# Performance work log

Hardware: AMD Instinct MI355X
Metric: run time of the kernel (lower is better)

The kernel has to match this reference:

```python
import jax, jax.numpy as jnp
import numpy as np

N = 100000          # nodes
E = 800000          # edges
H = 32              # hidden_features
L = 4               # num_layers
HS = 32             # hidden_edge_scores
EPS_BN = 1e-5
EPS_AGG = 1e-6


def _bn(x, g, b):
    # training-mode batch norm over the node/edge (batch) axis
    mu = jnp.mean(x, axis=0)
    var = jnp.var(x, axis=0)
    return (x - mu) * jax.lax.rsqrt(var + EPS_BN) * g + b


def setup_inputs() -> dict:
    key = jax.random.key(0)
    ks = jax.random.split(key, 24)
    rn = lambda k, s, sc=0.1: jax.random.normal(k, s, dtype=jnp.float32) * sc
    return {
        "x": rn(ks[0], (N, 1), 1.0),
        "e": rn(ks[1], (E, 1), 1.0),
        "edge_index": jax.random.randint(ks[2], (2, E), 0, N),
        # input projections
        "pe_w": rn(ks[3], (1, H)), "pe_b": rn(ks[4], (H,)),
        "ed_w": rn(ks[5], (1, H)), "ed_b": rn(ks[6], (H,)),
        # per-layer GatedGCN weights, stacked over layers
        "A_w": rn(ks[7], (L, H, H)), "A_b": rn(ks[8], (L, H)),
        "B_w": rn(ks[9], (L, H, H)), "B_b": rn(ks[10], (L, H)),
        "C_w": rn(ks[11], (L, H, H)), "C_b": rn(ks[12], (L, H)),
        "U_w": rn(ks[13], (L, H, H)), "U_b": rn(ks[14], (L, H)),
        "V_w": rn(ks[15], (L, H, H)), "V_b": rn(ks[16], (L, H)),
        # batch-norm affine params
        "bn_h_g": jnp.ones((L, H), jnp.float32), "bn_h_b": jnp.zeros((L, H), jnp.float32),
        "bn_e_g": jnp.ones((L, H), jnp.float32), "bn_e_b": jnp.zeros((L, H), jnp.float32),
        # score predictor: concat(src_h, dst_h, e) -> HS -> 1
        "W1_w": rn(ks[17], (3 * H, HS)), "W1_b": rn(ks[18], (HS,)),
        "W2_w": rn(ks[19], (HS, 1)), "W2_b": rn(ks[20], (1,)),
    }


def reference(x, e, edge_index, pe_w, pe_b, ed_w, ed_b,
              A_w, A_b, B_w, B_b, C_w, C_b, U_w, U_b, V_w, V_b,
              bn_h_g, bn_h_b, bn_e_g, bn_e_b, W1_w, W1_b, W2_w, W2_b):
    src, dst = edge_index[0], edge_index[1]
    h = x @ pe_w + pe_b          # [N, H]
    e = e @ ed_w + ed_b          # [E, H]
    n = h.shape[0]
    for l in range(L):
        Ah = h @ A_w[l] + A_b[l]
        Bh = h @ B_w[l] + B_b[l]
        Ce = e @ C_w[l] + C_b[l]
        Uh = h @ U_w[l] + U_b[l]
        Vh = h @ V_w[l] + V_b[l]
        # edge update: gather node features to edges
        e_new = Ah[dst] + Bh[src] + Ce               # [E, H]
        sigma = jax.nn.sigmoid(e_new)                # edge gates
        # gated mean aggregation: scatter-add to dst nodes
        num = jax.ops.segment_sum(sigma * Vh[src], dst, num_segments=n)
        den = jax.ops.segment_sum(sigma, dst, num_segments=n)
        h_new = Uh + num / (den + EPS_AGG)           # [N, H]
        # BN -> ReLU -> residual
        h = h + jax.nn.relu(_bn(h_new, bn_h_g[l], bn_h_b[l]))
        e = e + jax.nn.relu(_bn(e_new, bn_e_g[l], bn_e_b[l]))
    # score predictor over edges
    z = jnp.concatenate([h[src], h[dst], e], axis=1)  # [E, 3H]
    scores = jax.nn.relu(z @ W1_w + W1_b) @ W2_w + W2_b  # [E, 1]
    return scores
```

## Files before the change

kernel.cpp:

```cpp
#include <hip/hip_runtime.h>
#include <hip/hip_bf16.h>
#include <hip/hip_fp16.h>

#define NLAYERS 4
#define GRID_STRIDE 2048

typedef _Float16 half8_t __attribute__((ext_vector_type(8)));
typedef float float4_t __attribute__((ext_vector_type(4)));
typedef float float8_t __attribute__((ext_vector_type(8)));

__global__ void zero_ints(int* __restrict__ p, int n)
{
    int i = blockIdx.x * 256 + threadIdx.x;
    if (i < n) p[i] = 0;
}

__global__ void hist_kernel(const int* __restrict__ dsts, int* __restrict__ counts, int E)
{
    int i = blockIdx.x * 256 + threadIdx.x;
    if (i < E) atomicAdd(&counts[dsts[i]], 1);
}

__global__ __launch_bounds__(256) void scan1(const int* __restrict__ counts,
                                             int* __restrict__ offsets,
                                             int* __restrict__ blocksums, int N)
{
    __shared__ int sdata[256];
    int t = threadIdx.x;
    int bbase = blockIdx.x * 1024;
    int v[4]; int s = 0;
#pragma unroll
    for (int q = 0; q < 4; q++) {
        int idx = bbase + t * 4 + q;
        v[q] = (idx < N) ? counts[idx] : 0;
        s += v[q];
    }
    sdata[t] = s;
    __syncthreads();
    for (int off = 1; off < 256; off <<= 1) {
        int x = (t >= off) ? sdata[t - off] : 0;
        __syncthreads();
        sdata[t] += x;
        __syncthreads();
    }
    int excl = sdata[t] - s;
    int run = excl;
#pragma unroll
    for (int q = 0; q < 4; q++) {
        int idx = bbase + t * 4 + q;
        if (idx < N) offsets[idx] = run;
        run += v[q];
    }
    if (t == 255) blocksums[blockIdx.x] = sdata[255];
}

__global__ void scan2(int* __restrict__ blocksums, int nb)
{
    if (threadIdx.x == 0 && blockIdx.x == 0) {
        int run = 0;
        for (int b = 0; b < nb; b++) { int t = blocksums[b]; blocksums[b] = run; run += t; }
    }
}

__global__ void scan3(int* __restrict__ offsets, const int* __restrict__ blocksums,
                      int* __restrict__ cursor, int N)
{
    int i = blockIdx.x * 256 + threadIdx.x;
    if (i < N) {
        int v = offsets[i] + blocksums[i >> 10];
        offsets[i] = v;
        cursor[i] = v;
    }
}

__global__ void scatter_perm(const int* __restrict__ dsts, int* __restrict__ cursor,
                             int* __restrict__ perm, int* __restrict__ pos, int E, int N)
{
    int g = blockIdx.x & 7;
    int lo = (int)((long long)N * g >> 3);
    int hi = (int)((long long)N * (g + 1) >> 3);
    int nbg = gridDim.x >> 3;
    int bg = blockIdx.x >> 3;
    for (int i = bg * 256 + threadIdx.x; i < E; i += nbg * 256) {
        int d = dsts[i];
        if (d >= lo && d < hi) {
            int slot = atomicAdd(&cursor[d], 1);
            perm[slot] = i;
            pos[i] = slot;
        }
    }
}

__global__ void gather_sd(const int* __restrict__ perm, const int* __restrict__ srcs,
                          const int* __restrict__ dsts, int* __restrict__ srcp,
                          int* __restrict__ dstp, int E)
{
    int i = blockIdx.x * 256 + threadIdx.x;
    if (i < E) {
        int e = perm[i];
        srcp[i] = srcs[e];
        dstp[i] = dsts[e];
    }
}

__global__ void init_proj4(const float* __restrict__ in, const float* __restrict__ w,
                           const float* __restrict__ b, float4* __restrict__ out, size_t n4)
{
    size_t i = (size_t)blockIdx.x * 256 + threadIdx.x;
    if (i < n4) {
        int j4 = (int)(i & 7) * 4;
        float xv = in[i >> 3];
        float4 wv = *(const float4*)(w + j4);
        float4 bv = *(const float4*)(b + j4);
        out[i] = make_float4(fmaf(xv, wv.x, bv.x), fmaf(xv, wv.y, bv.y),
                             fmaf(xv, wv.z, bv.z), fmaf(xv, wv.w, bv.w));
    }
}

__global__ void init_ep16(const float* __restrict__ e_in, const int* __restrict__ perm,
                          const float* __restrict__ w, const float* __restrict__ b,
                          __half2* __restrict__ out, size_t n4)
{
    size_t i = (size_t)blockIdx.x * 256 + threadIdx.x;
    if (i < n4) {
        int row = (int)(i >> 3);
        float xv = e_in[perm[row]];
        int j4 = (int)(i & 7) * 4;
        float4 wv = *(const float4*)(w + j4);
        float4 bv = *(const float4*)(b + j4);
        out[i * 2]     = __floats2half2_rn(fmaf(xv, wv.x, bv.x), fmaf(xv, wv.y, bv.y));
        out[i * 2 + 1] = __floats2half2_rn(fmaf(xv, wv.z, bv.z), fmaf(xv, wv.w, bv.w));
    }
}

template <int FUSE>
__global__ __launch_bounds__(256) void node_gemm(
    float* __restrict__ h, const float* __restrict__ hnew_in,
    const float* __restrict__ sc_h, const float* __restrict__ sh_h,
    const float* __restrict__ Aw, const float* __restrict__ Ab,
    const float* __restrict__ Bw, const float* __restrict__ Bb,
    const float* __restrict__ Uw, const float* __restrict__ Ub,
    const float* __restrict__ Vw, const float* __restrict__ Vb,
    __half* __restrict__ Ahh, __half* __restrict__ Bhh,
    float* __restrict__ Uhh, __half* __restrict__ Vhh, int N)
{
    int tid = threadIdx.x;
    int lane = tid & 63;
    int m = lane & 15, q = lane >> 4;
    half8_t bA0, bA1, bB0, bB1, bU0, bU1, bV0, bV1;
    float scq[8], shq[8];
#pragma unroll
    for (int i = 0; i < 8; i++) {
        int k = q * 8 + i;
        bA0[i] = (_Float16)Aw[k * 32 + m];  bA1[i] = (_Float16)Aw[k * 32 + m + 16];
        bB0[i] = (_Float16)Bw[k * 32 + m];  bB1[i] = (_Float16)Bw[k * 32 + m + 16];
        bU0[i] = (_Float16)Uw[k * 32 + m];  bU1[i] = (_Float16)Uw[k * 32 + m + 16];
        bV0[i] = (_Float16)Vw[k * 32 + m];  bV1[i] = (_Float16)Vw[k * 32 + m + 16];
        if (FUSE) { scq[i] = sc_h[k]; shq[i] = sh_h[k]; }
    }
    float ab0 = Ab[m], ab1 = Ab[m + 16];
    float bb0 = Bb[m], bb1 = Bb[m + 16];
    float ub0 = Ub[m], ub1 = Ub[m + 16];
    float vb0 = Vb[m], vb1 = Vb[m + 16];

    int ntile = (N + 15) >> 4;
    int wid = blockIdx.x * 4 + (tid >> 6);
    int nwave = gridDim.x * 4;
    for (int t = wid; t < ntile; t += nwave) {
        int base = t << 4;
        int arow = base + m;
        bool valid = arow < N;
        if (!valid) arow = N - 1;
        float8_t hv = *(const float8_t*)(h + (size_t)arow * 32 + q * 8);
        if (FUSE) {
            float8_t pv = *(const float8_t*)(hnew_in + (size_t)arow * 32 + q * 8);
#pragma unroll
            for (int i = 0; i < 8; i++)
                hv[i] += fmaxf(fmaf(pv[i], scq[i], shq[i]), 0.f);
            if (valid) *(float8_t*)(h + (size_t)arow * 32 + q * 8) = hv;
        }
        half8_t a;
#pragma unroll
        for (int i = 0; i < 8; i++) a[i] = (_Float16)hv[i];
        float4_t aA0 = __builtin_amdgcn_mfma_f32_16x16x32_f16(a, bA0, (float4_t){0,0,0,0}, 0, 0, 0);
        float4_t aA1 = __builtin_amdgcn_mfma_f32_16x16x32_f16(a, bA1, (float4_t){0,0,0,0}, 0, 0, 0);
        float4_t aB0 = __builtin_amdgcn_mfma_f32_16x16x32_f16(a, bB0, (float4_t){0,0,0,0}, 0, 0, 0);
        float4_t aB1 = __builtin_amdgcn_mfma_f32_16x16x32_f16(a, bB1, (float4_t){0,0,0,0}, 0, 0, 0);
        float4_t aU0 = __builtin_amdgcn_mfma_f32_16x16x32_f16(a, bU0, (float4_t){0,0,0,0}, 0, 0, 0);
        float4_t aU1 = __builtin_amdgcn_mfma_f32_16x16x32_f16(a, bU1, (float4_t){0,0,0,0}, 0, 0, 0);
        float4_t aV0 = __builtin_amdgcn_mfma_f32_16x16x32_f16(a, bV0, (float4_t){0,0,0,0}, 0, 0, 0);
        float4_t aV1 = __builtin_amdgcn_mfma_f32_16x16x32_f16(a, bV1, (float4_t){0,0,0,0}, 0, 0, 0);
#pragma unroll
        for (int reg = 0; reg < 4; reg++) {
            int node = base + q * 4 + reg;
            if (node < N) {
                size_t o = (size_t)node * 32;
                Ahh[o + m]      = __float2half_rn(aA0[reg] + ab0);
                Ahh[o + m + 16] = __float2half_rn(aA1[reg] + ab1);
                Bhh[o + m]      = __float2half_rn(aB0[reg] + bb0);
                Bhh[o + m + 16] = __float2half_rn(aB1[reg] + bb1);
                Vhh[o + m]      = __float2half_rn(aV0[reg] + vb0);
                Vhh[o + m + 16] = __float2half_rn(aV1[reg] + vb1);
                Uhh[o + m]      = aU0[reg] + ub0;
                Uhh[o + m + 16] = aU1[reg] + ub1;
            }
        }
    }
}

__global__ __launch_bounds__(256) void edge_en(
    const __half* __restrict__ ep,
    const int* __restrict__ srcp, const int* __restrict__ dstp,
    const __half* __restrict__ Ah, const __half* __restrict__ Bh,
    const float* __restrict__ Cw, const float* __restrict__ Cb,
    __half* __restrict__ enh, float* __restrict__ partial, int E)
{
    __shared__ float red[256];
    int tid = threadIdx.x;
    int lane = tid & 63;
    int m = lane & 15, q = lane >> 4;
    half8_t b0, b1;
#pragma unroll
    for (int i = 0; i < 8; i++) {
        int k = q * 8 + i;
        b0[i] = (_Float16)Cw[k * 32 + m];
        b1[i] = (_Float16)Cw[k * 32 + m + 16];
    }
    float cb0 = Cb[m], cb1 = Cb[m + 16];
    float es0 = 0.f, eq0 = 0.f, es1 = 0.f, eq1 = 0.f;

    int ntile = (E + 15) >> 4;
    int wid = blockIdx.x * 4 + (tid >> 6);
    int nwave = gridDim.x * 4;
    for (int t = wid; t < ntile; t += nwave) {
        int base = t << 4;
        int arow = base + m;
        if (arow >= E) arow = E - 1;
        half8_t a = *(const half8_t*)(ep + (size_t)arow * 32 + q * 8);
        float4_t acc0 = __builtin_amdgcn_mfma_f32_16x16x32_f16(a, b0, (float4_t){0.f,0.f,0.f,0.f}, 0, 0, 0);
        float4_t acc1 = __builtin_amdgcn_mfma_f32_16x16x32_f16(a, b1, (float4_t){0.f,0.f,0.f,0.f}, 0, 0, 0);
#pragma unroll
        for (int reg = 0; reg < 4; reg++) {
            int row = q * 4 + reg;
            int edge = base + row;
            if (edge < E) {
                int s = srcp[edge], d = dstp[edge];
                float ah0 = __half2float(Ah[(size_t)d * 32 + m]);
                float bh0 = __half2float(Bh[(size_t)s * 32 + m]);
                float ah1 = __half2float(Ah[(size_t)d * 32 + m + 16]);
                float bh1 = __half2float(Bh[(size_t)s * 32 + m + 16]);
                float en0 = acc0[reg] + cb0 + ah0 + bh0;
                float en1 = acc1[reg] + cb1 + ah1 + bh1;
                enh[(size_t)edge * 32 + m]      = __float2half_rn(en0);
                enh[(size_t)edge * 32 + m + 16] = __float2half_rn(en1);
                es0 += en0; eq0 += en0 * en0;
                es1 += en1; eq1 += en1 * en1;
            }
        }
    }
    float* p = partial + (size_t)blockIdx.x * 64;
    __syncthreads();
    red[tid] = es0;
    __syncthreads();
    if (tid < 16) {
        float s = 0.f;
#pragma unroll
        for (int w = 0; w < 4; w++)
#pragma unroll
            for (int k = 0; k < 4; k++) s += red[w * 64 + k * 16 + tid];
        p[tid] = s;
    }
    __syncthreads();
    red[tid] = es1;
    __syncthreads();
    if (tid < 16) {
        float s = 0.f;
#pragma unroll
        for (int w = 0; w < 4; w++)
#pragma unroll
            for (int k = 0; k < 4; k++) s += red[w * 64 + k * 16 + tid];
        p[16 + tid] = s;
    }
    __syncthreads();
    red[tid] = eq0;
    __syncthreads();
    if (tid < 16) {
        float s = 0.f;
#pragma unroll
        for (int w = 0; w < 4; w++)
#pragma unroll
            for (int k = 0; k < 4; k++) s += red[w * 64 + k * 16 + tid];
        p[32 + tid] = s;
    }
    __syncthreads();
    red[tid] = eq1;
    __syncthreads();
    if (tid < 16) {
        float s = 0.f;
#pragma unroll
        for (int w = 0; w < 4; w++)
#pragma unroll
            for (int k = 0; k < 4; k++) s += red[w * 64 + k * 16 + tid];
        p[48 + tid] = s;
    }
}

__global__ __launch_bounds__(256) void node_agg(
    const __half* __restrict__ enh, const int* __restrict__ srcp,
    const int* __restrict__ offsets, const int* __restrict__ counts,
    const __half* __restrict__ Vh, float* __restrict__ hnew,
    __half* __restrict__ ep, const float* __restrict__ sc_e, const float* __restrict__ sh_e,
    float* __restrict__ partial, int N)
{
    __shared__ float red[512];
    int tid = threadIdx.x, u = tid & 15, grp = tid >> 4;
    int c0 = 2 * u;
    float sc0 = sc_e[c0], sh0 = sh_e[c0];
    float sc1 = sc_e[c0 + 1], sh1 = sh_e[c0 + 1];
    float hs0 = 0.f, hq0 = 0.f, hs1 = 0.f, hq1 = 0.f;
    for (int nb0 = blockIdx.x * 16; nb0 < N; nb0 += gridDim.x * 16) {
        int node = nb0 + grp;
        if (node >= N) break;
        int start = offsets[node], len = counts[node];
        float num0 = 0.f, den0 = 0.f, num1 = 0.f, den1 = 0.f;
        int qq = 0;
        for (; qq + 2 <= len; qq += 2) {
            int p0 = start + qq, p1 = p0 + 1;
            int s0 = srcp[p0], s1 = srcp[p1];
            float2 en0 = __half22float2(*(const __half2*)(enh + (size_t)p0 * 32 + c0));
            float2 en1 = __half22float2(*(const __half2*)(enh + (size_t)p1 * 32 + c0));
            float2 vh0 = __half22float2(*(const __half2*)(Vh + (size_t)s0 * 32 + c0));
            float2 vh1 = __half22float2(*(const __half2*)(Vh + (size_t)s1 * 32 + c0));
            float2 e0 = __half22float2(*(const __half2*)(ep + (size_t)p0 * 32 + c0));
            float2 e1 = __half22float2(*(const __half2*)(ep + (size_t)p1 * 32 + c0));
            float sg00 = 1.f / (1.f + __expf(-en0.x)), sg01 = 1.f / (1.f + __expf(-en0.y));
            float sg10 = 1.f / (1.f + __expf(-en1.x)), sg11 = 1.f / (1.f + __expf(-en1.y));
            num0 = fmaf(sg00, vh0.x, num0); num1 = fmaf(sg01, vh0.y, num1);
            num0 = fmaf(sg10, vh1.x, num0); num1 = fmaf(sg11, vh1.y, num1);
            den0 += sg00 + sg10; den1 += sg01 + sg11;
            *(__half2*)(ep + (size_t)p0 * 32 + c0) = __floats2half2_rn(
                e0.x + fmaxf(fmaf(en0.x, sc0, sh0), 0.f),
                e0.y + fmaxf(fmaf(en0.y, sc1, sh1), 0.f));
            *(__half2*)(ep + (size_t)p1 * 32 + c0) = __floats2half2_rn(
                e1.x + fmaxf(fmaf(en1.x, sc0, sh0), 0.f),
                e1.y + fmaxf(fmaf(en1.y, sc1, sh1), 0.f));
        }
        if (qq < len) {
            int p0 = start + qq;
            int s0 = srcp[p0];
            float2 en0 = __half22float2(*(const __half2*)(enh + (size_t)p0 * 32 + c0));
            float2 vh0 = __half22float2(*(const __half2*)(Vh + (size_t)s0 * 32 + c0));
            float2 e0 = __half22float2(*(const __half2*)(ep + (size_t)p0 * 32 + c0));
            float sg00 = 1.f / (1.f + __expf(-en0.x)), sg01 = 1.f / (1.f + __expf(-en0.y));
            num0 = fmaf(sg00, vh0.x, num0); num1 = fmaf(sg01, vh0.y, num1);
            den0 += sg00; den1 += sg01;
            *(__half2*)(ep + (size_t)p0 * 32 + c0) = __floats2half2_rn(
                e0.x + fmaxf(fmaf(en0.x, sc0, sh0), 0.f),
                e0.y + fmaxf(fmaf(en0.y, sc1, sh1), 0.f));
        }
        size_t ho = (size_t)node * 32 + c0;
        float hv0 = hnew[ho]     + num0 / (den0 + 1e-6f);
        float hv1 = hnew[ho + 1] + num1 / (den1 + 1e-6f);
        *(float2*)(hnew + ho) = make_float2(hv0, hv1);
        hs0 += hv0; hq0 += hv0 * hv0;
        hs1 += hv1; hq1 += hv1 * hv1;
    }
    __syncthreads();
    red[tid] = hs0; red[256 + tid] = hs1;
    __syncthreads();
    float* p = partial + (size_t)blockIdx.x * 64;
    if (tid < 32) {
        int uu = tid >> 1, par = tid & 1;
        const float* r = red + par * 256;
        float s = 0.f;
#pragma unroll
        for (int g = 0; g < 16; g++) s += r[g * 16 + uu];
        p[tid] = s;
    }
    __syncthreads();
    red[tid] = hq0; red[256 + tid] = hq1;
    __syncthreads();
    if (tid < 32) {
        int uu = tid >> 1, par = tid & 1;
        const float* r = red + par * 256;
        float s = 0.f;
#pragma unroll
        for (int g = 0; g < 16; g++) s += r[g * 16 + uu];
        p[32 + tid] = s;
    }
}

__global__ __launch_bounds__(256) void stats_side(
    const float* __restrict__ partial, int nrows, double cnt,
    const float* __restrict__ g, const float* __restrict__ b,
    float* __restrict__ sc_out, float* __restrict__ sh_out)
{
    int j = blockIdx.x;
    __shared__ double rs[256], rq[256];
    double s = 0.0, q = 0.0;
    for (int r = threadIdx.x; r < nrows; r += 256) {
        s += (double)partial[(size_t)r * 64 + j];
        q += (double)partial[(size_t)r * 64 + 32 + j];
    }
    rs[threadIdx.x] = s; rq[threadIdx.x] = q;
    __syncthreads();
    for (int off = 128; off; off >>= 1) {
        if (threadIdx.x < off) { rs[threadIdx.x] += rs[threadIdx.x + off]; rq[threadIdx.x] += rq[threadIdx.x + off]; }
        __syncthreads();
    }
    if (threadIdx.x == 0) {
        double mean = rs[0] / cnt;
        double var = rq[0] / cnt - mean * mean;
        float scale = g[j] * (float)(1.0 / sqrt(var + 1e-5));
        sc_out[j] = scale;
        sh_out[j] = b[j] - (float)mean * scale;
    }
}

__global__ void apply4_h16(const float4* __restrict__ pre, const float* __restrict__ scale,
                           const float* __restrict__ shift, const float4* __restrict__ hold,
                           __half2* __restrict__ h16, size_t n4)
{
    size_t i = (size_t)blockIdx.x * 256 + threadIdx.x;
    if (i < n4) {
        int j4 = (int)(i & 7) * 4;
        float4 sc = *(const float4*)(scale + j4);
        float4 sh = *(const float4*)(shift + j4);
        float4 p = pre[i], a = hold[i];
        a.x += fmaxf(fmaf(p.x, sc.x, sh.x), 0.f);
        a.y += fmaxf(fmaf(p.y, sc.y, sh.y), 0.f);
        a.z += fmaxf(fmaf(p.z, sc.z, sh.z), 0.f);
        a.w += fmaxf(fmaf(p.w, sc.w, sh.w), 0.f);
        h16[i * 2]     = __floats2half2_rn(a.x, a.y);
        h16[i * 2 + 1] = __floats2half2_rn(a.z, a.w);
    }
}

__global__ __launch_bounds__(256) void predictor(
    const __half* __restrict__ h16, const __half* __restrict__ e16,
    const int* __restrict__ srcs, const int* __restrict__ dsts, const int* __restrict__ pos,
    const float* __restrict__ W1, const float* __restrict__ b1,
    const float* __restrict__ W2, const float* __restrict__ b2v,
    float* __restrict__ out, int E)
{
    int tid = threadIdx.x;
    int lane = tid & 63;
    int m = lane & 15, q = lane >> 4;
    half8_t bf00, bf01, bf10, bf11, bf20, bf21;
#pragma unroll
    for (int i = 0; i < 8; i++) {
        int k = q * 8 + i;
        bf00[i] = (_Float16)W1[k * 32 + m];
        bf01[i] = (_Float16)W1[k * 32 + m + 16];
        bf10[i] = (_Float16)W1[(32 + k) * 32 + m];
        bf11[i] = (_Float16)W1[(32 + k) * 32 + m + 16];
        bf20[i] = (_Float16)W1[(64 + k) * 32 + m];
        bf21[i] = (_Float16)W1[(64 + k) * 32 + m + 16];
    }
    float b10 = b1[m], b11 = b1[m + 16];
    float w20 = W2[m], w21 = W2[m + 16];
    float b2 = b2v[0];

    int ntile = (E + 15) >> 4;
    int wid = blockIdx.x * 4 + (tid >> 6);
    int nwave = gridDim.x * 4;
    for (int t = wid; t < ntile; t += nwave) {
        int base = t << 4;
        int arow = base + m;
        if (arow >= E) arow = E - 1;
        int s = srcs[arow], d = dsts[arow];
        int erow = pos[arow];
        half8_t a0 = *(const half8_t*)(h16 + (size_t)s * 32 + q * 8);
        half8_t a1 = *(const half8_t*)(h16 + (size_t)d * 32 + q * 8);
        half8_t a2 = *(const half8_t*)(e16 + (size_t)erow * 32 + q * 8);
        float4_t acc0 = {0.f, 0.f, 0.f, 0.f}, acc1 = {0.f, 0.f, 0.f, 0.f};
        acc0 = __builtin_amdgcn_mfma_f32_16x16x32_f16(a0, bf00, acc0, 0, 0, 0);
        acc1 = __builtin_amdgcn_mfma_f32_16x16x32_f16(a0, bf01, acc1, 0, 0, 0);
        acc0 = __builtin_amdgcn_mfma_f32_16x16x32_f16(a1, bf10, acc0, 0, 0, 0);
        acc1 = __builtin_amdgcn_mfma_f32_16x16x32_f16(a1, bf11, acc1, 0, 0, 0);
        acc0 = __builtin_amdgcn_mfma_f32_16x16x32_f16(a2, bf20, acc0, 0, 0, 0);
        acc1 = __builtin_amdgcn_mfma_f32_16x16x32_f16(a2, bf21, acc1, 0, 0, 0);
#pragma unroll
        for (int reg = 0; reg < 4; reg++) {
            float tp = fmaxf(acc0[reg] + b10, 0.f) * w20
                     + fmaxf(acc1[reg] + b11, 0.f) * w21;
            tp += __shfl_xor(tp, 1);
            tp += __shfl_xor(tp, 2);
            tp += __shfl_xor(tp, 4);
            tp += __shfl_xor(tp, 8);
            int edge = base + q * 4 + reg;
            if (m == 0 && edge < E) out[edge] = tp + b2;
        }
    }
}

extern "C" void kernel_launch(void* const* d_in, const int* in_sizes, int n_in,
                              void* d_out, int out_size, void* d_ws, size_t ws_size,
                              hipStream_t stream)
{
    const int N = in_sizes[0];
    const int E = in_sizes[1];

    const float* x    = (const float*)d_in[0];
    const float* e_in = (const float*)d_in[1];
    const int*   eidx = (const int*)d_in[2];
    const float* pe_w = (const float*)d_in[3];
    const float* pe_b = (const float*)d_in[4];
    const float* ed_w = (const float*)d_in[5];
    const float* ed_b = (const float*)d_in[6];
    const float* Aw = (const float*)d_in[7];
    const float* Ab = (const float*)d_in[8];
    const float* Bw = (const float*)d_in[9];
    const float* Bb = (const float*)d_in[10];
    const float* Cw = (const float*)d_in[11];
    const float* Cb = (const float*)d_in[12];
    const float* Uw = (const float*)d_in[13];
    const float* Ub = (const float*)d_in[14];
    const float* Vw = (const float*)d_in[15];
    const float* Vb = (const float*)d_in[16];
    const float* bn_h_g = (const float*)d_in[17];
    const float* bn_h_b = (const float*)d_in[18];
    const float* bn_e_g = (const float*)d_in[19];
    const float* bn_e_b = (const float*)d_in[20];
    const float* W1w = (const float*)d_in[21];
    const float* W1b = (const float*)d_in[22];
    const float* W2w = (const float*)d_in[23];
    const float* W2b = (const float*)d_in[24];

    const int* srcs = eidx;
    const int* dsts = eidx + E;

    size_t nh = (size_t)N * 32;
    size_t eh = (size_t)E * 32;

    float* ws = (float*)d_ws;
    float* stats     = ws;
    float* partial_h = stats + 128;
    float* partial_e = partial_h + GRID_STRIDE * 64;
    float* h    = partial_e + GRID_STRIDE * 64;
    float* hnew = h + nh;
    __half* Ah  = (__half*)(hnew + nh);
    __half* Bh  = Ah + nh;
    __half* Vh  = Bh + nh;
    __half* ep  = Vh + nh;
    __half* enh = ep + eh;
    int* counts    = (int*)(enh + eh);
    int* offsets   = counts + N;
    int* cursor    = offsets + N;
    int* blocksums = cursor + N;
    int* perm      = blocksums + 128;
    int* srcp      = perm + E;
    int* dstp      = srcp + E;
    int* pos       = dstp + E;

    size_t nh4 = nh / 4, eh4 = eh / 4;
    int gh4 = (int)((nh4 + 255) / 256);
    int ge4 = (int)((eh4 + 255) / 256);
    int gN = (N + 255) / 256;
    int gE = (E + 255) / 256;
    int nb = (N + 1023) / 1024;
    int ntileN = (N + 15) / 16;
    int gGemm = (ntileN + 3) / 4;
    if (gGemm > GRID_STRIDE) gGemm = GRID_STRIDE;

    zero_ints<<<gN, 256, 0, stream>>>(counts, N);
    hist_kernel<<<gE, 256, 0, stream>>>(dsts, counts, E);
    scan1<<<nb, 256, 0, stream>>>(counts, offsets, blocksums, N);
    scan2<<<1, 64, 0, stream>>>(blocksums, nb);
    scan3<<<gN, 256, 0, stream>>>(offsets, blocksums, cursor, N);
    scatter_perm<<<GRID_STRIDE, 256, 0, stream>>>(dsts, cursor, perm, pos, E, N);
    gather_sd<<<gE, 256, 0, stream>>>(perm, srcs, dsts, srcp, dstp, E);

    init_proj4<<<gh4, 256, 0, stream>>>(x, pe_w, pe_b, (float4*)h, nh4);
    init_ep16<<<ge4, 256, 0, stream>>>(e_in, perm, ed_w, ed_b, (__half2*)ep, eh4);

    for (int l = 0; l < NLAYERS; l++) {
        if (l == 0)
            node_gemm<0><<<gGemm, 256, 0, stream>>>(h, hnew, stats + 0, stats + 32,
                Aw + l * 1024, Ab + l * 32, Bw + l * 1024, Bb + l * 32,
                Uw + l * 1024, Ub + l * 32, Vw + l * 1024, Vb + l * 32,
                Ah, Bh, hnew, Vh, N);
        else
            node_gemm<1><<<gGemm, 256, 0, stream>>>(h, hnew, stats + 0, stats + 32,
                Aw + l * 1024, Ab + l * 32, Bw + l * 1024, Bb + l * 32,
                Uw + l * 1024, Ub + l * 32, Vw + l * 1024, Vb + l * 32,
                Ah, Bh, hnew, Vh, N);
        edge_en<<<GRID_STRIDE, 256, 0, stream>>>(ep, srcp, dstp, Ah, Bh,
            Cw + l * 1024, Cb + l * 32, enh, partial_e, E);
        stats_side<<<32, 256, 0, stream>>>(partial_e, GRID_STRIDE, (double)E,
            bn_e_g + l * 32, bn_e_b + l * 32, stats + 64, stats + 96);
        node_agg<<<GRID_STRIDE, 256, 0, stream>>>(enh, srcp, offsets, counts,
            Vh, hnew, ep, stats + 64, stats + 96, partial_h, N);
        stats_side<<<32, 256, 0, stream>>>(partial_h, GRID_STRIDE, (double)N,
            bn_h_g + l * 32, bn_h_b + l * 32, stats + 0, stats + 32);
    }

    apply4_h16<<<gh4, 256, 0, stream>>>((const float4*)hnew, stats + 0, stats + 32,
                                        (const float4*)h, (__half2*)Ah, nh4);

    predictor<<<GRID_STRIDE, 256, 0, stream>>>((const __half*)Ah, (const __half*)ep,
                                               srcs, dsts, pos, W1w, W1b, W2w, W2b,
                                               (float*)d_out, E);
}
```

Baseline: 714.1 us.

## Fuse edge update and node aggregation into one dst-sorted kernel with deferred edge BN

Merges the per-edge C-projection and the gated aggregation into one kernel that walks dst-sorted edges per node. The edge residual update from the previous layer's BN is deferred and applied while the next layer reads the edge features; the last layer's update is applied inside the predictor. B and V are interleaved into one buffer so a single source gather fetches both, and the two stats kernels per layer become one. The aim is to cut enh/ep memory round-trips, the dstp index stream and launches. In exchange the Ce GEMM moves from MFMA to scalar FMAs driven by shuffles, which adds ALU work per edge.

```diff
diff --git a/kernel.cpp b/kernel.cpp
--- a/kernel.cpp
+++ b/kernel.cpp
@@ -91,16 +91,11 @@
     }
 }
 
-__global__ void gather_sd(const int* __restrict__ perm, const int* __restrict__ srcs,
-                          const int* __restrict__ dsts, int* __restrict__ srcp,
-                          int* __restrict__ dstp, int E)
+__global__ void gather_s(const int* __restrict__ perm, const int* __restrict__ srcs,
+                         int* __restrict__ srcp, int E)
 {
     int i = blockIdx.x * 256 + threadIdx.x;
-    if (i < E) {
-        int e = perm[i];
-        srcp[i] = srcs[e];
-        dstp[i] = dsts[e];
-    }
+    if (i < E) srcp[i] = srcs[perm[i]];
 }
 
 __global__ void init_proj4(const float* __restrict__ in, const float* __restrict__ w,
@@ -141,8 +136,8 @@
     const float* __restrict__ Bw, const float* __restrict__ Bb,
     const float* __restrict__ Uw, const float* __restrict__ Ub,
     const float* __restrict__ Vw, const float* __restrict__ Vb,
-    __half* __restrict__ Ahh, __half* __restrict__ Bhh,
-    float* __restrict__ Uhh, __half* __restrict__ Vhh, int N)
+    __half* __restrict__ Ahh, __half* __restrict__ BVh,
+    float* __restrict__ Uhh, int N)
 {
     int tid = threadIdx.x;
     int lane = tid & 63;
@@ -194,191 +189,111 @@
         for (int reg = 0; reg < 4; reg++) {
             int node = base + q * 4 + reg;
             if (node < N) {
-                size_t o = (size_t)node * 32;
-                Ahh[o + m]      = __float2half_rn(aA0[reg] + ab0);
-                Ahh[o + m + 16] = __float2half_rn(aA1[reg] + ab1);
-                Bhh[o + m]      = __float2half_rn(aB0[reg] + bb0);
-                Bhh[o + m + 16] = __float2half_rn(aB1[reg] + bb1);
-                Vhh[o + m]      = __float2half_rn(aV0[reg] + vb0);
-                Vhh[o + m + 16] = __float2half_rn(aV1[reg] + vb1);
-                Uhh[o + m]      = aU0[reg] + ub0;
-                Uhh[o + m + 16] = aU1[reg] + ub1;
+                size_t o  = (size_t)node * 32;
+                size_t o2 = (size_t)node * 64;
+                Ahh[o + m]       = __float2half_rn(aA0[reg] + ab0);
+                Ahh[o + m + 16]  = __float2half_rn(aA1[reg] + ab1);
+                BVh[o2 + m]      = __float2half_rn(aB0[reg] + bb0);
+                BVh[o2 + m + 16] = __float2half_rn(aB1[reg] + bb1);
+                BVh[o2 + 32 + m] = __float2half_rn(aV0[reg] + vb0);
+                BVh[o2 + 48 + m] = __float2half_rn(aV1[reg] + vb1);
+                Uhh[o + m]       = aU0[reg] + ub0;
+                Uhh[o + m + 16]  = aU1[reg] + ub1;
             }
         }
     }
 }
 
-__global__ __launch_bounds__(256) void edge_en(
-    const __half* __restrict__ ep,
-    const int* __restrict__ srcp, const int* __restrict__ dstp,
-    const __half* __restrict__ Ah, const __half* __restrict__ Bh,
+template <int FIRST>
+__global__ __launch_bounds__(256) void fused_edge_node(
+    const int* __restrict__ srcp, const int* __restrict__ offsets,
+    const int* __restrict__ counts,
+    const __half* __restrict__ Ahh, const __half* __restrict__ BVh,
+    __half* __restrict__ ep, __half* __restrict__ enh,
     const float* __restrict__ Cw, const float* __restrict__ Cb,
-    __half* __restrict__ enh, float* __restrict__ partial, int E)
-{
-    __shared__ float red[256];
-    int tid = threadIdx.x;
-    int lane = tid & 63;
-    int m = lane & 15, q = lane >> 4;
-    half8_t b0, b1;
-#pragma unroll
-    for (int i = 0; i < 8; i++) {
-        int k = q * 8 + i;
-        b0[i] = (_Float16)Cw[k * 32 + m];
-        b1[i] = (_Float16)Cw[k * 32 + m + 16];
-    }
-    float cb0 = Cb[m], cb1 = Cb[m + 16];
-    float es0 = 0.f, eq0 = 0.f, es1 = 0.f, eq1 = 0.f;
-
-    int ntile = (E + 15) >> 4;
-    int wid = blockIdx.x * 4 + (tid >> 6);
-    int nwave = gridDim.x * 4;
-    for (int t = wid; t < ntile; t += nwave) {
-        int base = t << 4;
-        int arow = base + m;
-        if (arow >= E) arow = E - 1;
-        half8_t a = *(const half8_t*)(ep + (size_t)arow * 32 + q * 8);
-        float4_t acc0 = __builtin_amdgcn_mfma_f32_16x16x32_f16(a, b0, (float4_t){0.f,0.f,0.f,0.f}, 0, 0, 0);
-        float4_t acc1 = __builtin_amdgcn_mfma_f32_16x16x32_f16(a, b1, (float4_t){0.f,0.f,0.f,0.f}, 0, 0, 0);
-#pragma unroll
-        for (int reg = 0; reg < 4; reg++) {
-            int row = q * 4 + reg;
-            int edge = base + row;
-            if (edge < E) {
-                int s = srcp[edge], d = dstp[edge];
-                float ah0 = __half2float(Ah[(size_t)d * 32 + m]);
-                float bh0 = __half2float(Bh[(size_t)s * 32 + m]);
-                float ah1 = __half2float(Ah[(size_t)d * 32 + m + 16]);
-                float bh1 = __half2float(Bh[(size_t)s * 32 + m + 16]);
-                float en0 = acc0[reg] + cb0 + ah0 + bh0;
-                float en1 = acc1[reg] + cb1 + ah1 + bh1;
-                enh[(size_t)edge * 32 + m]      = __float2half_rn(en0);
-                enh[(size_t)edge * 32 + m + 16] = __float2half_rn(en1);
-                es0 += en0; eq0 += en0 * en0;
-                es1 += en1; eq1 += en1 * en1;
-            }
-        }
-    }
-    float* p = partial + (size_t)blockIdx.x * 64;
-    __syncthreads();
-    red[tid] = es0;
-    __syncthreads();
-    if (tid < 16) {
-        float s = 0.f;
-#pragma unroll
-        for (int w = 0; w < 4; w++)
-#pragma unroll
-            for (int k = 0; k < 4; k++) s += red[w * 64 + k * 16 + tid];
-        p[tid] = s;
-    }
-    __syncthreads();
-    red[tid] = es1;
-    __syncthreads();
-    if (tid < 16) {
-        float s = 0.f;
-#pragma unroll
-        for (int w = 0; w < 4; w++)
-#pragma unroll
-            for (int k = 0; k < 4; k++) s += red[w * 64 + k * 16 + tid];
-        p[16 + tid] = s;
-    }
-    __syncthreads();
-    red[tid] = eq0;
-    __syncthreads();
-    if (tid < 16) {
-        float s = 0.f;
-#pragma unroll
-        for (int w = 0; w < 4; w++)
-#pragma unroll
-            for (int k = 0; k < 4; k++) s += red[w * 64 + k * 16 + tid];
-        p[32 + tid] = s;
-    }
-    __syncthreads();
-    red[tid] = eq1;
-    __syncthreads();
-    if (tid < 16) {
-        float s = 0.f;
-#pragma unroll
-        for (int w = 0; w < 4; w++)
-#pragma unroll
-            for (int k = 0; k < 4; k++) s += red[w * 64 + k * 16 + tid];
-        p[48 + tid] = s;
-    }
-}
-
-__global__ __launch_bounds__(256) void node_agg(
-    const __half* __restrict__ enh, const int* __restrict__ srcp,
-    const int* __restrict__ offsets, const int* __restrict__ counts,
-    const __half* __restrict__ Vh, float* __restrict__ hnew,
-    __half* __restrict__ ep, const float* __restrict__ sc_e, const float* __restrict__ sh_e,
-    float* __restrict__ partial, int N)
+    const float* __restrict__ sc_e, const float* __restrict__ sh_e,
+    float* __restrict__ hnew, float* __restrict__ partial, int N)
 {
     __shared__ float red[512];
     int tid = threadIdx.x, u = tid & 15, grp = tid >> 4;
     int c0 = 2 * u;
-    float sc0 = sc_e[c0], sh0 = sh_e[c0];
-    float sc1 = sc_e[c0 + 1], sh1 = sh_e[c0 + 1];
+    float4 cw[16];
+#pragma unroll
+    for (int t = 0; t < 16; t++) {
+        float2 w0 = *(const float2*)(Cw + (2 * t) * 32 + c0);
+        float2 w1 = *(const float2*)(Cw + (2 * t + 1) * 32 + c0);
+        cw[t] = make_float4(w0.x, w0.y, w1.x, w1.y);
+    }
+    float cb0 = Cb[c0], cb1 = Cb[c0 + 1];
+    float sce0 = 0.f, she0 = 0.f, sce1 = 0.f, she1 = 0.f;
+    if (!FIRST) {
+        sce0 = sc_e[c0];     she0 = sh_e[c0];
+        sce1 = sc_e[c0 + 1]; she1 = sh_e[c0 + 1];
+    }
+    float es0 = 0.f, eq0 = 0.f, es1 = 0.f, eq1 = 0.f;
     float hs0 = 0.f, hq0 = 0.f, hs1 = 0.f, hq1 = 0.f;
+
     for (int nb0 = blockIdx.x * 16; nb0 < N; nb0 += gridDim.x * 16) {
         int node = nb0 + grp;
         if (node >= N) break;
         int start = offsets[node], len = counts[node];
+        float2 ah = __half22float2(*(const __half2*)(Ahh + (size_t)node * 32 + c0));
+        float base0 = cb0 + ah.x, base1 = cb1 + ah.y;
         float num0 = 0.f, den0 = 0.f, num1 = 0.f, den1 = 0.f;
-        int qq = 0;
-        for (; qq + 2 <= len; qq += 2) {
-            int p0 = start + qq, p1 = p0 + 1;
-            int s0 = srcp[p0], s1 = srcp[p1];
-            float2 en0 = __half22float2(*(const __half2*)(enh + (size_t)p0 * 32 + c0));
-            float2 en1 = __half22float2(*(const __half2*)(enh + (size_t)p1 * 32 + c0));
-            float2 vh0 = __half22float2(*(const __half2*)(Vh + (size_t)s0 * 32 + c0));
-            float2 vh1 = __half22float2(*(const __half2*)(Vh + (size_t)s1 * 32 + c0));
-            float2 e0 = __half22float2(*(const __half2*)(ep + (size_t)p0 * 32 + c0));
-            float2 e1 = __half22float2(*(const __half2*)(ep + (size_t)p1 * 32 + c0));
-            float sg00 = 1.f / (1.f + __expf(-en0.x)), sg01 = 1.f / (1.f + __expf(-en0.y));
-            float sg10 = 1.f / (1.f + __expf(-en1.x)), sg11 = 1.f / (1.f + __expf(-en1.y));
-            num0 = fmaf(sg00, vh0.x, num0); num1 = fmaf(sg01, vh0.y, num1);
-            num0 = fmaf(sg10, vh1.x, num0); num1 = fmaf(sg11, vh1.y, num1);
-            den0 += sg00 + sg10; den1 += sg01 + sg11;
-            *(__half2*)(ep + (size_t)p0 * 32 + c0) = __floats2half2_rn(
-                e0.x + fmaxf(fmaf(en0.x, sc0, sh0), 0.f),
-                e0.y + fmaxf(fmaf(en0.y, sc1, sh1), 0.f));
-            *(__half2*)(ep + (size_t)p1 * 32 + c0) = __floats2half2_rn(
-                e1.x + fmaxf(fmaf(en1.x, sc0, sh0), 0.f),
-                e1.y + fmaxf(fmaf(en1.y, sc1, sh1), 0.f));
-        }
-        if (qq < len) {
-            int p0 = start + qq;
-            int s0 = srcp[p0];
-            float2 en0 = __half22float2(*(const __half2*)(enh + (size_t)p0 * 32 + c0));
-            float2 vh0 = __half22float2(*(const __half2*)(Vh + (size_t)s0 * 32 + c0));
-            float2 e0 = __half22float2(*(const __half2*)(ep + (size_t)p0 * 32 + c0));
-            float sg00 = 1.f / (1.f + __expf(-en0.x)), sg01 = 1.f / (1.f + __expf(-en0.y));
-            num0 = fmaf(sg00, vh0.x, num0); num1 = fmaf(sg01, vh0.y, num1);
-            den0 += sg00; den1 += sg01;
-            *(__half2*)(ep + (size_t)p0 * 32 + c0) = __floats2half2_rn(
-                e0.x + fmaxf(fmaf(en0.x, sc0, sh0), 0.f),
-                e0.y + fmaxf(fmaf(en0.y, sc1, sh1), 0.f));
+        for (int qq = 0; qq < len; qq++) {
+            int p = start + qq;
+            int s = srcp[p];
+            const __half2* bv = (const __half2*)(BVh + (size_t)s * 64);
+            float2 bh = __half22float2(bv[u]);
+            float2 vh = __half22float2(bv[16 + u]);
+            float2 ev = __half22float2(*(const __half2*)(ep + (size_t)p * 32 + c0));
+            if (!FIRST) {
+                float2 enp = __half22float2(*(const __half2*)(enh + (size_t)p * 32 + c0));
+                ev.x += fmaxf(fmaf(enp.x, sce0, she0), 0.f);
+                ev.y += fmaxf(fmaf(enp.y, sce1, she1), 0.f);
+                *(__half2*)(ep + (size_t)p * 32 + c0) = __floats2half2_rn(ev.x, ev.y);
+            }
+            float a0 = base0 + bh.x, a1 = base1 + bh.y;
+#pragma unroll
+            for (int t = 0; t < 16; t++) {
+                float e0 = __shfl(ev.x, t, 16);
+                float e1 = __shfl(ev.y, t, 16);
+                a0 = fmaf(e0, cw[t].x, a0);
+                a0 = fmaf(e1, cw[t].z, a0);
+                a1 = fmaf(e0, cw[t].y, a1);
+                a1 = fmaf(e1, cw[t].w, a1);
+            }
+            *(__half2*)(enh + (size_t)p * 32 + c0) = __floats2half2_rn(a0, a1);
+            es0 += a0; eq0 += a0 * a0;
+            es1 += a1; eq1 += a1 * a1;
+            float sg0 = 1.f / (1.f + __expf(-a0));
+            float sg1 = 1.f / (1.f + __expf(-a1));
+            num0 = fmaf(sg0, vh.x, num0); num1 = fmaf(sg1, vh.y, num1);
+            den0 += sg0; den1 += sg1;
         }
         size_t ho = (size_t)node * 32 + c0;
-        float hv0 = hnew[ho]     + num0 / (den0 + 1e-6f);
-        float hv1 = hnew[ho + 1] + num1 / (den1 + 1e-6f);
+        float2 uh = *(const float2*)(hnew + ho);
+        float hv0 = uh.x + num0 / (den0 + 1e-6f);
+        float hv1 = uh.y + num1 / (den1 + 1e-6f);
         *(float2*)(hnew + ho) = make_float2(hv0, hv1);
         hs0 += hv0; hq0 += hv0 * hv0;
         hs1 += hv1; hq1 += hv1 * hv1;
     }
-    __syncthreads();
-    red[tid] = hs0; red[256 + tid] = hs1;
-    __syncthreads();
-    float* p = partial + (size_t)blockIdx.x * 64;
+
+    float* pp = partial + (size_t)blockIdx.x * 128;
+    __syncthreads();
+    red[tid] = es0; red[256 + tid] = es1;
+    __syncthreads();
     if (tid < 32) {
         int uu = tid >> 1, par = tid & 1;
         const float* r = red + par * 256;
         float s = 0.f;
 #pragma unroll
         for (int g = 0; g < 16; g++) s += r[g * 16 + uu];
-        p[tid] = s;
-    }
-    __syncthreads();
-    red[tid] = hq0; red[256 + tid] = hq1;
+        pp[tid] = s;
+    }
+    __syncthreads();
+    red[tid] = eq0; red[256 + tid] = eq1;
     __syncthreads();
     if (tid < 32) {
         int uu = tid >> 1, par = tid & 1;
@@ -386,21 +301,46 @@
         float s = 0.f;
 #pragma unroll
         for (int g = 0; g < 16; g++) s += r[g * 16 + uu];
-        p[32 + tid] = s;
-    }
-}
-
-__global__ __launch_bounds__(256) void stats_side(
-    const float* __restrict__ partial, int nrows, double cnt,
-    const float* __restrict__ g, const float* __restrict__ b,
-    float* __restrict__ sc_out, float* __restrict__ sh_out)
+        pp[32 + tid] = s;
+    }
+    __syncthreads();
+    red[tid] = hs0; red[256 + tid] = hs1;
+    __syncthreads();
+    if (tid < 32) {
+        int uu = tid >> 1, par = tid & 1;
+        const float* r = red + par * 256;
+        float s = 0.f;
+#pragma unroll
+        for (int g = 0; g < 16; g++) s += r[g * 16 + uu];
+        pp[64 + tid] = s;
+    }
+    __syncthreads();
+    red[tid] = hq0; red[256 + tid] = hq1;
+    __syncthreads();
+    if (tid < 32) {
+        int uu = tid >> 1, par = tid & 1;
+        const float* r = red + par * 256;
+        float s = 0.f;
+#pragma unroll
+        for (int g = 0; g < 16; g++) s += r[g * 16 + uu];
+        pp[96 + tid] = s;
+    }
+}
+
+__global__ __launch_bounds__(256) void stats_both(
+    const float* __restrict__ partial, int nrows, double cntE, double cntN,
+    const float* __restrict__ eg, const float* __restrict__ eb,
+    const float* __restrict__ hg, const float* __restrict__ hb,
+    float* __restrict__ stats)
 {
     int j = blockIdx.x;
+    int side = j >> 5, jj = j & 31;
     __shared__ double rs[256], rq[256];
     double s = 0.0, q = 0.0;
+    const float* base = partial + side * 64;
     for (int r = threadIdx.x; r < nrows; r += 256) {
-        s += (double)partial[(size_t)r * 64 + j];
-        q += (double)partial[(size_t)r * 64 + 32 + j];
+        s += (double)base[(size_t)r * 128 + jj];
+        q += (double)base[(size_t)r * 128 + 32 + jj];
     }
     rs[threadIdx.x] = s; rq[threadIdx.x] = q;
     __syncthreads();
@@ -409,11 +349,15 @@
         __syncthreads();
     }
     if (threadIdx.x == 0) {
+        double cnt = side ? cntN : cntE;
         double mean = rs[0] / cnt;
         double var = rq[0] / cnt - mean * mean;
-        float scale = g[j] * (float)(1.0 / sqrt(var + 1e-5));
-        sc_out[j] = scale;
-        sh_out[j] = b[j] - (float)mean * scale;
+        const float* g = side ? hg : eg;
+        const float* b = side ? hb : eb;
+        float scale = g[jj] * (float)(1.0 / sqrt(var + 1e-5));
+        int off2 = side ? 0 : 64;
+        stats[off2 + jj] = scale;
+        stats[off2 + 32 + jj] = b[jj] - (float)mean * scale;
     }
 }
 
@@ -437,8 +381,10 @@
 }
 
 __global__ __launch_bounds__(256) void predictor(
-    const __half* __restrict__ h16, const __half* __restrict__ e16,
+    const __half* __restrict__ h16, const __half* __restrict__ ep,
+    const __half* __restrict__ enh,
     const int* __restrict__ srcs, const int* __restrict__ dsts, const int* __restrict__ pos,
+    const float* __restrict__ sc_e, const float* __restrict__ sh_e,
     const float* __restrict__ W1, const float* __restrict__ b1,
     const float* __restrict__ W2, const float* __restrict__ b2v,
     float* __restrict__ out, int E)
@@ -447,6 +393,7 @@
     int lane = tid & 63;
     int m = lane & 15, q = lane >> 4;
     half8_t bf00, bf01, bf10, bf11, bf20, bf21;
+    float scq[8], shq[8];
 #pragma unroll
     for (int i = 0; i < 8; i++) {
         int k = q * 8 + i;
@@ -456,6 +403,7 @@
         bf11[i] = (_Float16)W1[(32 + k) * 32 + m + 16];
         bf20[i] = (_Float16)W1[(64 + k) * 32 + m];
         bf21[i] = (_Float16)W1[(64 + k) * 32 + m + 16];
+        scq[i] = sc_e[k]; shq[i] = sh_e[k];
     }
     float b10 = b1[m], b11 = b1[m + 16];
     float w20 = W2[m], w21 = W2[m + 16];
@@ -472,7 +420,14 @@
         int erow = pos[arow];
         half8_t a0 = *(const half8_t*)(h16 + (size_t)s * 32 + q * 8);
         half8_t a1 = *(const half8_t*)(h16 + (size_t)d * 32 + q * 8);
-        half8_t a2 = *(const half8_t*)(e16 + (size_t)erow * 32 + q * 8);
+        half8_t ee = *(const half8_t*)(ep + (size_t)erow * 32 + q * 8);
+        half8_t enr = *(const half8_t*)(enh + (size_t)erow * 32 + q * 8);
+        half8_t a2;
+#pragma unroll
+        for (int i = 0; i < 8; i++) {
+            float evv = (float)ee[i] + fmaxf(fmaf((float)enr[i], scq[i], shq[i]), 0.f);
+            a2[i] = (_Float16)evv;
+        }
         float4_t acc0 = {0.f, 0.f, 0.f, 0.f}, acc1 = {0.f, 0.f, 0.f, 0.f};
         acc0 = __builtin_amdgcn_mfma_f32_16x16x32_f16(a0, bf00, acc0, 0, 0, 0);
         acc1 = __builtin_amdgcn_mfma_f32_16x16x32_f16(a0, bf01, acc1, 0, 0, 0);
@@ -534,15 +489,13 @@
     size_t eh = (size_t)E * 32;
 
     float* ws = (float*)d_ws;
-    float* stats     = ws;
-    float* partial_h = stats + 128;
-    float* partial_e = partial_h + GRID_STRIDE * 64;
-    float* h    = partial_e + GRID_STRIDE * 64;
+    float* stats   = ws;
+    float* partial = stats + 128;
+    float* h    = partial + (size_t)GRID_STRIDE * 128;
     float* hnew = h + nh;
     __half* Ah  = (__half*)(hnew + nh);
-    __half* Bh  = Ah + nh;
-    __half* Vh  = Bh + nh;
-    __half* ep  = Vh + nh;
+    __half* BV  = Ah + nh;
+    __half* ep  = BV + 2 * nh;
     __half* enh = ep + eh;
     int* counts    = (int*)(enh + eh);
     int* offsets   = counts + N;
@@ -550,8 +503,7 @@
     int* blocksums = cursor + N;
     int* perm      = blocksums + 128;
     int* srcp      = perm + E;
-    int* dstp      = srcp + E;
-    int* pos       = dstp + E;
+    int* pos       = srcp + E;
 
     size_t nh4 = nh / 4, eh4 = eh / 4;
     int gh4 = (int)((nh4 + 255) / 256);
@@ -569,7 +521,7 @@
     scan2<<<1, 64, 0, stream>>>(blocksums, nb);
     scan3<<<gN, 256, 0, stream>>>(offsets, blocksums, cursor, N);
     scatter_perm<<<GRID_STRIDE, 256, 0, stream>>>(dsts, cursor, perm, pos, E, N);
-    gather_sd<<<gE, 256, 0, stream>>>(perm, srcs, dsts, srcp, dstp, E);
+    gather_s<<<gE, 256, 0, stream>>>(perm, srcs, srcp, E);
 
     init_proj4<<<gh4, 256, 0, stream>>>(x, pe_w, pe_b, (float4*)h, nh4);
     init_ep16<<<ge4, 256, 0, stream>>>(e_in, perm, ed_w, ed_b, (__half2*)ep, eh4);
@@ -579,26 +531,29 @@
             node_gemm<0><<<gGemm, 256, 0, stream>>>(h, hnew, stats + 0, stats + 32,
                 Aw + l * 1024, Ab + l * 32, Bw + l * 1024, Bb + l * 32,
                 Uw + l * 1024, Ub + l * 32, Vw + l * 1024, Vb + l * 32,
-                Ah, Bh, hnew, Vh, N);
+                Ah, BV, hnew, N);
         else
             node_gemm<1><<<gGemm, 256, 0, stream>>>(h, hnew, stats + 0, stats + 32,
                 Aw + l * 1024, Ab + l * 32, Bw + l * 1024, Bb + l * 32,
                 Uw + l * 1024, Ub + l * 32, Vw + l * 1024, Vb + l * 32,
-                Ah, Bh, hnew, Vh, N);
-        edge_en<<<GRID_STRIDE, 256, 0, stream>>>(ep, srcp, dstp, Ah, Bh,
-            Cw + l * 1024, Cb + l * 32, enh, partial_e, E);
-        stats_side<<<32, 256, 0, stream>>>(partial_e, GRID_STRIDE, (double)E,
-            bn_e_g + l * 32, bn_e_b + l * 32, stats + 64, stats + 96);
-        node_agg<<<GRID_STRIDE, 256, 0, stream>>>(enh, srcp, offsets, counts,
-            Vh, hnew, ep, stats + 64, stats + 96, partial_h, N);
-        stats_side<<<32, 256, 0, stream>>>(partial_h, GRID_STRIDE, (double)N,
-            bn_h_g + l * 32, bn_h_b + l * 32, stats + 0, stats + 32);
+                Ah, BV, hnew, N);
+        if (l == 0)
+            fused_edge_node<1><<<GRID_STRIDE, 256, 0, stream>>>(srcp, offsets, counts,
+                Ah, BV, ep, enh, Cw + l * 1024, Cb + l * 32,
+                stats + 64, stats + 96, hnew, partial, N);
+        else
+            fused_edge_node<0><<<GRID_STRIDE, 256, 0, stream>>>(srcp, offsets, counts,
+                Ah, BV, ep, enh, Cw + l * 1024, Cb + l * 32,
+                stats + 64, stats + 96, hnew, partial, N);
+        stats_both<<<64, 256, 0, stream>>>(partial, GRID_STRIDE, (double)E, (double)N,
+            bn_e_g + l * 32, bn_e_b + l * 32, bn_h_g + l * 32, bn_h_b + l * 32, stats);
     }
 
     apply4_h16<<<gh4, 256, 0, stream>>>((const float4*)hnew, stats + 0, stats + 32,
                                         (const float4*)h, (__half2*)Ah, nh4);
 
-    predictor<<<GRID_STRIDE, 256, 0, stream>>>((const __half*)Ah, (const __half*)ep,
-                                               srcs, dsts, pos, W1w, W1b, W2w, W2b,
+    predictor<<<GRID_STRIDE, 256, 0, stream>>>((const __half*)Ah, ep, enh,
+                                               srcs, dsts, pos, stats + 64, stats + 96,
+                                               W1w, W1b, W2w, W2b,
                                                (float*)d_out, E);
 }
```

After: 1.007 ms. 41.0% more time.

## Sort nodes by degree for aggregation and iterate predictor in dst-sorted edge order

Applied to the files above, without the earlier changes.

Adds a counting sort of nodes by in-degree (capped at 63) so that node_agg's 16-lane groups in a block process nodes of similar degree, reducing divergence and load imbalance within waves. The predictor now walks edges in the dst-sorted order, reading ep contiguously and scattering outputs through perm instead of gathering ep through pos, which also drops the pos array. This costs four small extra setup kernels and makes node_agg's reads of offsets and counts indirect and scattered.

```diff
diff --git a/kernel.cpp b/kernel.cpp
--- a/kernel.cpp
+++ b/kernel.cpp
@@ -74,7 +74,7 @@
 }
 
 __global__ void scatter_perm(const int* __restrict__ dsts, int* __restrict__ cursor,
-                             int* __restrict__ perm, int* __restrict__ pos, int E, int N)
+                             int* __restrict__ perm, int E, int N)
 {
     int g = blockIdx.x & 7;
     int lo = (int)((long long)N * g >> 3);
@@ -86,7 +86,6 @@
         if (d >= lo && d < hi) {
             int slot = atomicAdd(&cursor[d], 1);
             perm[slot] = i;
-            pos[i] = slot;
         }
     }
 }
@@ -100,6 +99,34 @@
         int e = perm[i];
         srcp[i] = srcs[e];
         dstp[i] = dsts[e];
+    }
+}
+
+__global__ void deg_hist(const int* __restrict__ counts, int* __restrict__ dhist, int N)
+{
+    int i = blockIdx.x * 256 + threadIdx.x;
+    if (i < N) {
+        int d = counts[i]; if (d > 63) d = 63;
+        atomicAdd(&dhist[d], 1);
+    }
+}
+
+__global__ void deg_scan(const int* __restrict__ dhist, int* __restrict__ dcur)
+{
+    if (threadIdx.x == 0 && blockIdx.x == 0) {
+        int run = 0;
+        for (int b = 0; b < 64; b++) { int t = dhist[b]; dcur[b] = run; run += t; }
+    }
+}
+
+__global__ void deg_scatter(const int* __restrict__ counts, int* __restrict__ dcur,
+                            int* __restrict__ nodeord, int N)
+{
+    int i = blockIdx.x * 256 + threadIdx.x;
+    if (i < N) {
+        int d = counts[i]; if (d > 63) d = 63;
+        int slot = atomicAdd(&dcur[d], 1);
+        nodeord[slot] = i;
     }
 }
 
@@ -308,6 +335,7 @@
 __global__ __launch_bounds__(256) void node_agg(
     const __half* __restrict__ enh, const int* __restrict__ srcp,
     const int* __restrict__ offsets, const int* __restrict__ counts,
+    const int* __restrict__ nodeord,
     const __half* __restrict__ Vh, float* __restrict__ hnew,
     __half* __restrict__ ep, const float* __restrict__ sc_e, const float* __restrict__ sh_e,
     float* __restrict__ partial, int N)
@@ -319,8 +347,9 @@
     float sc1 = sc_e[c0 + 1], sh1 = sh_e[c0 + 1];
     float hs0 = 0.f, hq0 = 0.f, hs1 = 0.f, hq1 = 0.f;
     for (int nb0 = blockIdx.x * 16; nb0 < N; nb0 += gridDim.x * 16) {
-        int node = nb0 + grp;
-        if (node >= N) break;
+        int slot = nb0 + grp;
+        if (slot >= N) break;
+        int node = nodeord[slot];
         int start = offsets[node], len = counts[node];
         float num0 = 0.f, den0 = 0.f, num1 = 0.f, den1 = 0.f;
         int qq = 0;
@@ -438,7 +467,7 @@
 
 __global__ __launch_bounds__(256) void predictor(
     const __half* __restrict__ h16, const __half* __restrict__ e16,
-    const int* __restrict__ srcs, const int* __restrict__ dsts, const int* __restrict__ pos,
+    const int* __restrict__ srcp, const int* __restrict__ dstp, const int* __restrict__ perm,
     const float* __restrict__ W1, const float* __restrict__ b1,
     const float* __restrict__ W2, const float* __restrict__ b2v,
     float* __restrict__ out, int E)
@@ -468,11 +497,10 @@
         int base = t << 4;
         int arow = base + m;
         if (arow >= E) arow = E - 1;
-        int s = srcs[arow], d = dsts[arow];
-        int erow = pos[arow];
+        int s = srcp[arow], d = dstp[arow];
         half8_t a0 = *(const half8_t*)(h16 + (size_t)s * 32 + q * 8);
         half8_t a1 = *(const half8_t*)(h16 + (size_t)d * 32 + q * 8);
-        half8_t a2 = *(const half8_t*)(e16 + (size_t)erow * 32 + q * 8);
+        half8_t a2 = *(const half8_t*)(e16 + (size_t)arow * 32 + q * 8);
         float4_t acc0 = {0.f, 0.f, 0.f, 0.f}, acc1 = {0.f, 0.f, 0.f, 0.f};
         acc0 = __builtin_amdgcn_mfma_f32_16x16x32_f16(a0, bf00, acc0, 0, 0, 0);
         acc1 = __builtin_amdgcn_mfma_f32_16x16x32_f16(a0, bf01, acc1, 0, 0, 0);
@@ -488,8 +516,11 @@
             tp += __shfl_xor(tp, 2);
             tp += __shfl_xor(tp, 4);
             tp += __shfl_xor(tp, 8);
-            int edge = base + q * 4 + reg;
-            if (m == 0 && edge < E) out[edge] = tp + b2;
+            int idx = base + q * 4 + reg;
+            if (m == 0 && idx < E) {
+                int oe = perm[idx];
+                out[oe] = tp + b2;
+            }
         }
     }
 }
@@ -551,7 +582,9 @@
     int* perm      = blocksums + 128;
     int* srcp      = perm + E;
     int* dstp      = srcp + E;
-    int* pos       = dstp + E;
+    int* nodeord   = dstp + E;
+    int* dhist     = nodeord + N;
+    int* dcur      = dhist + 64;
 
     size_t nh4 = nh / 4, eh4 = eh / 4;
     int gh4 = (int)((nh4 + 255) / 256);
@@ -565,10 +598,14 @@
 
     zero_ints<<<gN, 256, 0, stream>>>(counts, N);
     hist_kernel<<<gE, 256, 0, stream>>>(dsts, counts, E);
+    zero_ints<<<1, 256, 0, stream>>>(dhist, 64);
+    deg_hist<<<gN, 256, 0, stream>>>(counts, dhist, N);
+    deg_scan<<<1, 64, 0, stream>>>(dhist, dcur);
+    deg_scatter<<<gN, 256, 0, stream>>>(counts, dcur, nodeord, N);
     scan1<<<nb, 256, 0, stream>>>(counts, offsets, blocksums, N);
     scan2<<<1, 64, 0, stream>>>(blocksums, nb);
     scan3<<<gN, 256, 0, stream>>>(offsets, blocksums, cursor, N);
-    scatter_perm<<<GRID_STRIDE, 256, 0, stream>>>(dsts, cursor, perm, pos, E, N);
+    scatter_perm<<<GRID_STRIDE, 256, 0, stream>>>(dsts, cursor, perm, E, N);
     gather_sd<<<gE, 256, 0, stream>>>(perm, srcs, dsts, srcp, dstp, E);
 
     init_proj4<<<gh4, 256, 0, stream>>>(x, pe_w, pe_b, (float4*)h, nh4);
@@ -589,7 +626,7 @@
             Cw + l * 1024, Cb + l * 32, enh, partial_e, E);
         stats_side<<<32, 256, 0, stream>>>(partial_e, GRID_STRIDE, (double)E,
             bn_e_g + l * 32, bn_e_b + l * 32, stats + 64, stats + 96);
-        node_agg<<<GRID_STRIDE, 256, 0, stream>>>(enh, srcp, offsets, counts,
+        node_agg<<<GRID_STRIDE, 256, 0, stream>>>(enh, srcp, offsets, counts, nodeord,
             Vh, hnew, ep, stats + 64, stats + 96, partial_h, N);
         stats_side<<<32, 256, 0, stream>>>(partial_h, GRID_STRIDE, (double)N,
             bn_h_g + l * 32, bn_h_b + l * 32, stats + 0, stats + 32);
@@ -599,6 +636,6 @@
                                         (const float4*)h, (__half2*)Ah, nh4);
 
     predictor<<<GRID_STRIDE, 256, 0, stream>>>((const __half*)Ah, (const __half*)ep,
-                                               srcs, dsts, pos, W1w, W1b, W2w, W2b,
+                                               srcp, dstp, perm, W1w, W1b, W2w, W2b,
                                                (float*)d_out, E);
 }
```

After: 1.409 ms. 97.3% more time.
